# Kernel tuning notes

Measured on AMD Instinct MI355X. Metric: run time of the kernel, lower is better.

The kernel has to match this reference:

```python
import jax, jax.numpy as jnp
import numpy as np

DIM = 1024
HEADS = 16
DIM_HEADS = DIM // HEADS  # 64
DIM_HIDDEN = DIM_HEADS * HEADS


def setup_inputs() -> dict:
    key = jax.random.key(0)
    k1, k2, k3, k4, k5 = jax.random.split(key, 5)
    b, t = 2, 2048
    x = jax.random.normal(k1, (b, t, DIM), dtype=jnp.float32)
    # torch nn.Linear weights are [out_features, in_features]
    s = DIM ** -0.5
    W_q = jax.random.normal(k2, (DIM_HIDDEN, DIM), dtype=jnp.float32) * s
    W_kv = jax.random.normal(k3, (2 * DIM_HIDDEN, DIM), dtype=jnp.float32) * s
    W_out = jax.random.normal(k4, (DIM, DIM_HIDDEN), dtype=jnp.float32) * s
    b_out = jax.random.normal(k5, (DIM,), dtype=jnp.float32) * 0.01
    return {"x": x, "W_q": W_q, "W_kv": W_kv, "W_out": W_out, "b_out": b_out}


def reference(x, W_q, W_kv, W_out, b_out):
    b, t, d = x.shape
    h, e = HEADS, DIM_HEADS
    # projections (Linear: x @ W.T)
    q = jnp.einsum('btd,fd->btf', x, W_q)
    kv = jnp.einsum('btd,fd->btf', x, W_kv)
    k, v = jnp.split(kv, 2, axis=-1)
    # split heads -> (b, h, t, e)
    split = lambda z: z.reshape(b, t, h, e).transpose(0, 2, 1, 3)
    q, k, v = split(q), split(k), split(v)
    # scaled dot-product attention; original uses exp/sum/div softmax
    scores = jnp.einsum('bhqe,bhke->bhqk', q, k) * (e ** -0.5)
    attn = jax.nn.softmax(scores, axis=-1)
    out = jnp.einsum('bhqk,bhke->bhqe', attn, v)
    out = out.transpose(0, 2, 1, 3).reshape(b, t, h * e)
    return jnp.einsum('btf,df->btd', out, W_out) + b_out
```

## Files before the change

### kernel.cpp

```cpp
#include <hip/hip_runtime.h>
#include <hip/hip_bf16.h>

#define BB   2
#define TT   2048
#define DD   1024
#define HH   16
#define EE   64
#define BT   4096

typedef __attribute__((ext_vector_type(8))) short bf16x8;
typedef __attribute__((ext_vector_type(4))) float floatx4;
typedef __attribute__((ext_vector_type(16))) float floatx16;

__device__ __forceinline__ unsigned short f2bf(float f) {
  unsigned int x = __float_as_uint(f);
  x += 0x7fffu + ((x >> 16) & 1u);
  return (unsigned short)(x >> 16);
}
__device__ __forceinline__ unsigned int pack2u(float a, float b) {
  union { __hip_bfloat162 h; unsigned int u; } r;
  r.h = __float22bfloat162_rn(make_float2(a, b));
  return r.u;
}
__device__ __forceinline__ uint4 pack8(const float4& a, const float4& b) {
  union { uint4 u; __hip_bfloat162 h[4]; } r;
  r.h[0] = __float22bfloat162_rn(make_float2(a.x, a.y));
  r.h[1] = __float22bfloat162_rn(make_float2(a.z, a.w));
  r.h[2] = __float22bfloat162_rn(make_float2(b.x, b.y));
  r.h[3] = __float22bfloat162_rn(make_float2(b.z, b.w));
  return r.u;
}
__device__ __forceinline__ void ld16(unsigned short* lds, const unsigned short* g) {
  __builtin_amdgcn_global_load_lds(
      (const __attribute__((address_space(1))) unsigned int*)g,
      (__attribute__((address_space(3))) unsigned int*)lds, 16, 0, 0);
}

#define GX   524288
#define GWQ  131072
#define GWKV 262144
#define GWO  131072

__global__ __launch_bounds__(256) void convert_kernel(
    const float* __restrict__ X,  const float* __restrict__ Wq,
    const float* __restrict__ Wkv, const float* __restrict__ Wout,
    unsigned short* __restrict__ Xb, unsigned short* __restrict__ Wb,
    unsigned short* __restrict__ Wob) {
  int g = blockIdx.x * 256 + threadIdx.x;
  const float* src; unsigned short* dst; int gi;
  if (g < GX)                        { src = X;    dst = Xb;  gi = g; }
  else if ((g -= GX) < GWQ)          { src = Wq;   dst = Wb;  gi = g; }
  else if ((g -= GWQ) < GWKV)        { src = Wkv;  dst = Wb + (size_t)GWQ * 8; gi = g; }
  else                               { src = Wout; dst = Wob; gi = g - GWKV; }
  const float4* s4 = reinterpret_cast<const float4*>(src) + (size_t)gi * 2;
  float4 a = s4[0], b = s4[1];
  reinterpret_cast<uint4*>(dst)[gi] = pack8(a, b);
}

__global__ __launch_bounds__(256) void gemm_qkv_mfma(
    const unsigned short* __restrict__ Xb,
    const unsigned short* __restrict__ Wb,
    unsigned short* __restrict__ Qh,
    unsigned short* __restrict__ Kh,
    unsigned short* __restrict__ Vt) {
  __shared__ __align__(16) unsigned short smem[128 * 136];
  unsigned short* As = smem;
  unsigned short* Bs = smem + 128 * 64;
  const int tid  = threadIdx.x;
  const int lane = tid & 63, w = tid >> 6;
  const int wm = w >> 1, wn = w & 1;
  const int q = lane >> 4, c = lane & 15;
  const int bm0 = blockIdx.y * 128;
  const int bn0 = blockIdx.x * 128;
  const unsigned short* Ag = Xb + (size_t)bm0 * DD;
  const unsigned short* Bg = Wb + (size_t)bn0 * DD;

  floatx4 acc[4][4];
#pragma unroll
  for (int i = 0; i < 4; ++i)
#pragma unroll
    for (int j = 0; j < 4; ++j) acc[i][j] = (floatx4){0.f, 0.f, 0.f, 0.f};

  int prow[4], pch[4];
#pragma unroll
  for (int t = 0; t < 4; ++t) {
    int s = (w * 4 + t) * 64 + lane;
    prow[t] = s >> 3;
    pch[t]  = (s & 7) ^ (prow[t] & 7);
  }
  int aoff[4][2], boff[4][2];
#pragma unroll
  for (int i = 0; i < 4; ++i)
#pragma unroll
    for (int h = 0; h < 2; ++h) {
      aoff[i][h] = (wm * 64 + i * 16 + c) * 64 + (((q + h * 4) ^ (c & 7)) << 3);
      boff[i][h] = (wn * 64 + i * 16 + c) * 64 + (((q + h * 4) ^ (c & 7)) << 3);
    }

  for (int kk = 0; kk < DD; kk += 64) {
    __syncthreads();
#pragma unroll
    for (int t = 0; t < 4; ++t) {
      int i = w * 4 + t;
      ld16(&As[i * 512], &Ag[(size_t)prow[t] * DD + kk + pch[t] * 8]);
      ld16(&Bs[i * 512], &Bg[(size_t)prow[t] * DD + kk + pch[t] * 8]);
    }
    __syncthreads();
    bf16x8 af[4][2], bfr[4][2];
#pragma unroll
    for (int i = 0; i < 4; ++i)
#pragma unroll
      for (int h = 0; h < 2; ++h) {
        af[i][h]  = *reinterpret_cast<const bf16x8*>(&As[aoff[i][h]]);
        bfr[i][h] = *reinterpret_cast<const bf16x8*>(&Bs[boff[i][h]]);
      }
#pragma unroll
    for (int i = 0; i < 4; ++i)
#pragma unroll
      for (int j = 0; j < 4; ++j) {
        acc[i][j] = __builtin_amdgcn_mfma_f32_16x16x32_bf16(af[i][0], bfr[j][0], acc[i][j], 0, 0, 0);
        acc[i][j] = __builtin_amdgcn_mfma_f32_16x16x32_bf16(af[i][1], bfr[j][1], acc[i][j], 0, 0, 0);
      }
  }

  const int region = bn0 >> 10;
  if (region < 2) {
    const float scl = (region == 0) ? 0.18033688011112042f : 1.0f;
    __syncthreads();
    unsigned short* tb = smem;
#pragma unroll
    for (int i = 0; i < 4; ++i) {
#pragma unroll
      for (int j = 0; j < 4; ++j) {
        int n  = wn * 64 + j * 16 + c;
        int m0 = wm * 64 + i * 16 + q * 4;
#pragma unroll
        for (int reg = 0; reg < 4; ++reg)
          tb[(m0 + reg) * 136 + n] = f2bf(acc[i][j][reg] * scl);
      }
    }
    __syncthreads();
    unsigned short* dst = (region == 0) ? Qh : Kh;
    const int b   = bm0 >> 11;
    const int t0  = bm0 & 2047;
    const int nb0 = bn0 & 1023;
    const int oct = tid & 15;
    const int nb  = nb0 + oct * 8;
    const int h   = nb >> 6, e = nb & 63;
#pragma unroll
    for (int it = 0; it < 8; ++it) {
      int tr = it * 16 + (tid >> 4);
      uint4 vv = *reinterpret_cast<const uint4*>(&tb[tr * 136 + oct * 8]);
      *reinterpret_cast<uint4*>(
          &dst[((size_t)((b * HH + h) * TT + t0 + tr)) * EE + e]) = vv;
    }
  } else {
    __syncthreads();
    unsigned short* tb = smem;
#pragma unroll
    for (int i = 0; i < 4; ++i) {
#pragma unroll
      for (int j = 0; j < 4; ++j) {
        int nl = wn * 64 + j * 16 + c;
        int ml = wm * 64 + i * 16 + q * 4;
        ushort4 pk;
        pk.x = f2bf(acc[i][j][0]);
        pk.y = f2bf(acc[i][j][1]);
        pk.z = f2bf(acc[i][j][2]);
        pk.w = f2bf(acc[i][j][3]);
        *reinterpret_cast<ushort4*>(&tb[nl * 136 + ml]) = pk;
      }
    }
    __syncthreads();
    const int b  = bm0 >> 11;
    const int t0 = bm0 & 2047;
    const int nb0 = bn0 & 1023;
    const int lr = tid & 15;
#pragma unroll
    for (int it = 0; it < 8; ++it) {
      int nl = it * 16 + (tid >> 4);
      int nb = nb0 + nl;
      int h = nb >> 6, e = nb & 63;
      uint4 vv = *reinterpret_cast<const uint4*>(&tb[nl * 136 + lr * 8]);
      *reinterpret_cast<uint4*>(
          &Vt[((size_t)(b * HH + h) * EE + e) * TT + t0 + lr * 8]) = vv;
    }
  }
}

#define NKT 32

#define ATILE(P, PREF, VMC)                                                    \
  do {                                                                         \
    if (PREF) {                                                                \
      _Pragma("unroll")                                                        \
      for (int t = 0; t < 4; ++t) {                                            \
        ld16(&Kbuf[((P) ^ 1) * 4096 + (t * 2 + w) * 512], kpre[t]);            \
        kpre[t] += 4096;                                                       \
        ld16(&Vbuf[((P) ^ 1) * 4096 + (t * 2 + w) * 512], vpre[t]);            \
        vpre[t] += 64;                                                         \
      }                                                                        \
    }                                                                          \
    asm volatile("s_waitcnt vmcnt(" VMC ")" ::: "memory");                     \
    asm volatile("s_barrier" ::: "memory");                                    \
    bf16x8 kf[2][4];                                                           \
    _Pragma("unroll")                                                          \
    for (int nt = 0; nt < 2; ++nt)                                             \
      _Pragma("unroll")                                                        \
      for (int kc = 0; kc < 4; ++kc)                                           \
        kf[nt][kc] = *reinterpret_cast<const bf16x8*>(                         \
            &Kbuf[(P) * 4096 + koff[nt][kc]]);                                 \
    floatx16 sacc[2];                                                          \
    __builtin_amdgcn_s_setprio(1);                                             \
    _Pragma("unroll")                                                          \
    for (int nt = 0; nt < 2; ++nt) {                                           \
      sacc[nt] = __builtin_amdgcn_mfma_f32_32x32x16_bf16(kf[nt][0], qf[0], zf, 0, 0, 0); \
      _Pragma("unroll")                                                        \
      for (int kc = 1; kc < 4; ++kc)                                           \
        sacc[nt] = __builtin_amdgcn_mfma_f32_32x32x16_bf16(kf[nt][kc], qf[kc], sacc[nt], 0, 0, 0); \
    }                                                                          \
    __builtin_amdgcn_s_setprio(0);                                             \
    unsigned int pp[2][8];                                                     \
    _Pragma("unroll")                                                          \
    for (int nt = 0; nt < 2; ++nt)                                             \
      _Pragma("unroll")                                                        \
      for (int r = 0; r < 8; ++r) {                                            \
        float e0 = __builtin_amdgcn_exp2f(sacc[nt][2 * r]);                    \
        float e1 = __builtin_amdgcn_exp2f(sacc[nt][2 * r + 1]);                \
        pp[nt][r] = pack2u(e0, e1);                                            \
      }                                                                        \
    __builtin_amdgcn_s_setprio(1);                                             \
    _Pragma("unroll")                                                          \
    for (int nt = 0; nt < 2; ++nt)                                             \
      _Pragma("unroll")                                                        \
      for (int kcp = 0; kcp < 2; ++kcp) {                                      \
        union { unsigned int u[4]; bf16x8 v; } pf;                             \
        pf.u[0] = pp[nt][4 * kcp + 0]; pf.u[1] = pp[nt][4 * kcp + 1];          \
        pf.u[2] = pp[nt][4 * kcp + 2]; pf.u[3] = pp[nt][4 * kcp + 3];          \
        lacc = __builtin_amdgcn_mfma_f32_32x32x16_bf16(pf.v, onesf.v, lacc, 0, 0, 0); \
        _Pragma("unroll")                                                      \
        for (int eh = 0; eh < 2; ++eh) {                                       \
          const int cc = nt * 4 + 2 * kcp;                                     \
          uint2 v0 = *reinterpret_cast<const uint2*>(                          \
              &Vbuf[(P) * 4096 + voff[eh][cc]]);                               \
          uint2 v1 = *reinterpret_cast<const uint2*>(                          \
              &Vbuf[(P) * 4096 + voff[eh][cc + 1]]);                           \
          union { unsigned int u[4]; bf16x8 v; } vf;                           \
          vf.u[0] = v0.x; vf.u[1] = v0.y; vf.u[2] = v1.x; vf.u[3] = v1.y;      \
          o_acc[eh] = __builtin_amdgcn_mfma_f32_32x32x16_bf16(pf.v, vf.v, o_acc[eh], 0, 0, 0); \
        }                                                                      \
      }                                                                        \
    __builtin_amdgcn_s_setprio(0);                                             \
    asm volatile("s_barrier" ::: "memory");                                    \
  } while (0)

__global__ __launch_bounds__(128) void attn_kernel(
    const unsigned short* __restrict__ Qh,
    const unsigned short* __restrict__ Kh,
    const unsigned short* __restrict__ Vtg,
    unsigned short* __restrict__ Aw) {
  __shared__ __align__(16) unsigned short smem[16384];

  const int tid  = threadIdx.x;
  const int lane = tid & 63;
  const int w    = tid >> 6;
  const int n31  = lane & 31;
  const int g    = lane >> 5;

  const int flat = blockIdx.y * 32 + blockIdx.x;
  const int idx  = flat >> 3;
  const int bh   = (flat & 7) * 4 + (idx >> 5);
  const int qt   = idx & 31;
  const size_t base = (size_t)bh * TT * EE;
  const unsigned short* Qp = Qh + base + (size_t)(qt * 64 + w * 32) * EE;
  const unsigned short* Kp = Kh + base;
  const unsigned short* Vp = Vtg + base;

  unsigned short* Kbuf = smem;
  unsigned short* Vbuf = smem + 8192;

  union { unsigned int u[4]; bf16x8 v; } onesf;
  onesf.u[0] = 0x3F803F80u; onesf.u[1] = 0x3F803F80u;
  onesf.u[2] = 0x3F803F80u; onesf.u[3] = 0x3F803F80u;

  const floatx16 zf = (floatx16)(0.0f);

  bf16x8 qf[4];
#pragma unroll
  for (int kc = 0; kc < 4; ++kc)
    qf[kc] = *reinterpret_cast<const bf16x8*>(
        &Qp[(size_t)n31 * EE + kc * 16 + g * 8]);

  int srow[4], sch[4];
#pragma unroll
  for (int t = 0; t < 4; ++t) {
    int s = (t * 2 + w) * 64 + lane;
    srow[t] = s >> 3;
    sch[t]  = (s & 7) ^ (srow[t] & 7);
  }

  int koff[2][4];
#pragma unroll
  for (int nt = 0; nt < 2; ++nt) {
    const int krow = nt * 32 + n31;
#pragma unroll
    for (int kc = 0; kc < 4; ++kc)
      koff[nt][kc] = krow * 64 + (((kc * 2 + g) ^ (krow & 7)) << 3);
  }
  int voff[2][8];
#pragma unroll
  for (int eh = 0; eh < 2; ++eh) {
    const int vrow = eh * 32 + n31;
#pragma unroll
    for (int cc = 0; cc < 8; ++cc)
      voff[eh][cc] = vrow * 64 + ((cc ^ (vrow & 7)) << 3) + g * 4;
  }

  const unsigned short* kpre[4];
  const unsigned short* vpre[4];
#pragma unroll
  for (int t = 0; t < 4; ++t) {
    kpre[t] = Kp + (size_t)(64 + srow[t]) * EE + sch[t] * 8;
    vpre[t] = Vp + (size_t)srow[t] * TT + 64 + sch[t] * 8;
  }

  floatx16 o_acc[2];
  o_acc[0] = (floatx16)(0.0f);
  o_acc[1] = (floatx16)(0.0f);
  floatx16 lacc = (floatx16)(0.0f);

#pragma unroll
  for (int t = 0; t < 4; ++t) {
    ld16(&Kbuf[(t * 2 + w) * 512], Kp + (size_t)srow[t] * EE + sch[t] * 8);
    ld16(&Vbuf[(t * 2 + w) * 512], Vp + (size_t)srow[t] * TT + sch[t] * 8);
  }

  for (int kt2 = 0; kt2 < 15; ++kt2) {
    ATILE(0, true, "8");
    ATILE(1, true, "8");
  }
  ATILE(0, true, "8");
  ATILE(1, false, "0");

  const int b = bh >> 4, h = bh & 15;
#pragma unroll
  for (int eh = 0; eh < 2; ++eh)
#pragma unroll
    for (int reg = 0; reg < 16; ++reg) {
      int qrl = (reg & 3) + 8 * (reg >> 2) + 4 * g;
      int t = qt * 64 + w * 32 + qrl;
      Aw[((size_t)(b * TT + t)) * DD + h * EE + eh * 32 + n31] =
          f2bf(o_acc[eh][reg] * (1.0f / lacc[reg]));
    }
}

__global__ __launch_bounds__(256) void gemm_out_mfma(
    const unsigned short* __restrict__ A,
    const unsigned short* __restrict__ Wob,
    const float* __restrict__ bias,
    float* __restrict__ out) {
  __shared__ __align__(16) unsigned short As[128 * 64];
  __shared__ __align__(16) unsigned short Bs[64 * 64];
  const int tid  = threadIdx.x;
  const int lane = tid & 63, w = tid >> 6;
  const int wm = w >> 1, wn = w & 1;
  const int q = lane >> 4, c = lane & 15;
  const int bm0 = blockIdx.y * 128;
  const int bn0 = blockIdx.x * 64;
  const unsigned short* Ag = A + (size_t)bm0 * DD;
  const unsigned short* Bg = Wob + (size_t)bn0 * DD;

  floatx4 acc[4][2];
#pragma unroll
  for (int i = 0; i < 4; ++i)
#pragma unroll
    for (int j = 0; j < 2; ++j) acc[i][j] = (floatx4){0.f, 0.f, 0.f, 0.f};

  int parow[4], pach[4];
#pragma unroll
  for (int t = 0; t < 4; ++t) {
    int s = (w * 4 + t) * 64 + lane;
    parow[t] = s >> 3;
    pach[t]  = (s & 7) ^ (parow[t] & 7);
  }
  int pbrow[2], pbch[2];
#pragma unroll
  for (int t = 0; t < 2; ++t) {
    int s = (w * 2 + t) * 64 + lane;
    pbrow[t] = s >> 3;
    pbch[t]  = (s & 7) ^ (pbrow[t] & 7);
  }

  for (int kk = 0; kk < DD; kk += 64) {
    __syncthreads();
#pragma unroll
    for (int t = 0; t < 4; ++t)
      ld16(&As[(w * 4 + t) * 512], &Ag[(size_t)parow[t] * DD + kk + pach[t] * 8]);
#pragma unroll
    for (int t = 0; t < 2; ++t)
      ld16(&Bs[(w * 2 + t) * 512], &Bg[(size_t)pbrow[t] * DD + kk + pbch[t] * 8]);
    __syncthreads();
    bf16x8 af[4][2], bfr[2][2];
#pragma unroll
    for (int h = 0; h < 2; ++h) {
      int ksw = ((q + h * 4) ^ (c & 7)) << 3;
#pragma unroll
      for (int i = 0; i < 4; ++i)
        af[i][h] = *reinterpret_cast<const bf16x8*>(&As[(wm * 64 + i * 16 + c) * 64 + ksw]);
#pragma unroll
      for (int j = 0; j < 2; ++j)
        bfr[j][h] = *reinterpret_cast<const bf16x8*>(&Bs[(wn * 32 + j * 16 + c) * 64 + ksw]);
    }
#pragma unroll
    for (int i = 0; i < 4; ++i)
#pragma unroll
      for (int j = 0; j < 2; ++j) {
        acc[i][j] = __builtin_amdgcn_mfma_f32_16x16x32_bf16(af[i][0], bfr[j][0], acc[i][j], 0, 0, 0);
        acc[i][j] = __builtin_amdgcn_mfma_f32_16x16x32_bf16(af[i][1], bfr[j][1], acc[i][j], 0, 0, 0);
      }
  }

#pragma unroll
  for (int i = 0; i < 4; ++i) {
#pragma unroll
    for (int j = 0; j < 2; ++j) {
      int n = bn0 + wn * 32 + j * 16 + c;
      float bv = bias[n];
#pragma unroll
      for (int reg = 0; reg < 4; ++reg) {
        int m = bm0 + wm * 64 + i * 16 + q * 4 + reg;
        out[(size_t)m * DD + n] = acc[i][j][reg] + bv;
      }
    }
  }
}

extern "C" void kernel_launch(void* const* d_in, const int* in_sizes, int n_in,
                              void* d_out, int out_size, void* d_ws, size_t ws_size,
                              hipStream_t stream) {
  const float* X    = (const float*)d_in[0];
  const float* Wq   = (const float*)d_in[1];
  const float* Wkv  = (const float*)d_in[2];
  const float* Wout = (const float*)d_in[3];
  const float* bout = (const float*)d_in[4];
  float* out = (float*)d_out;

  unsigned short* Qh  = (unsigned short*)d_ws;
  unsigned short* Kh  = Qh + (size_t)BT * DD;
  unsigned short* Vt  = Kh + (size_t)BT * DD;
  unsigned short* Aw  = Vt + (size_t)BT * DD;
  unsigned short* Xb  = Aw;
  unsigned short* Wb  = Aw + (size_t)BT * DD;
  unsigned short* Wob = Wb + (size_t)3 * 1024 * DD;

  convert_kernel<<<dim3(4096), 256, 0, stream>>>(X, Wq, Wkv, Wout, Xb, Wb, Wob);
  gemm_qkv_mfma<<<dim3(24, 32), 256, 0, stream>>>(Xb, Wb, Qh, Kh, Vt);
  attn_kernel<<<dim3(32, 32), 128, 0, stream>>>(Qh, Kh, Vt, Aw);
  gemm_out_mfma<<<dim3(16, 32), 256, 0, stream>>>(Aw, Wob, bout, out);
}
```

Measured before the change: 194.4 us.

## Stage V tiles through registers into a padded LDS layout

V tiles are now loaded from global memory into registers and written to LDS with a padded row stride of 68 elements, replacing the XOR-swizzled direct global-to-LDS loads. The V-operand reads in the PV MFMA loop use plain padded offsets. The aim is to cut LDS bank conflicts on the 8-byte V fragment reads. In exchange it adds VGPR pressure, explicit ds_write instructions and an extra vmcnt/lgkmcnt wait inside each tile, so the V load latency has to be hidden within a single tile's compute.

```diff
diff --git a/kernel.cpp b/kernel.cpp
--- a/kernel.cpp
+++ b/kernel.cpp
@@ -189,16 +189,20 @@
 }
 
 #define NKT 32
+#define VST 68
 
 #define ATILE(P, PREF, VMC)                                                    \
   do {                                                                         \
     if (PREF) {                                                                \
       _Pragma("unroll")                                                        \
       for (int t = 0; t < 4; ++t) {                                            \
+        vreg[t] = *reinterpret_cast<const uint4*>(vpre[t]);                    \
+        vpre[t] += 64;                                                         \
+      }                                                                        \
+      _Pragma("unroll")                                                        \
+      for (int t = 0; t < 4; ++t) {                                            \
         ld16(&Kbuf[((P) ^ 1) * 4096 + (t * 2 + w) * 512], kpre[t]);            \
         kpre[t] += 4096;                                                       \
-        ld16(&Vbuf[((P) ^ 1) * 4096 + (t * 2 + w) * 512], vpre[t]);            \
-        vpre[t] += 64;                                                         \
       }                                                                        \
     }                                                                          \
     asm volatile("s_waitcnt vmcnt(" VMC ")" ::: "memory");                     \
@@ -242,15 +246,25 @@
         for (int eh = 0; eh < 2; ++eh) {                                       \
           const int cc = nt * 4 + 2 * kcp;                                     \
           uint2 v0 = *reinterpret_cast<const uint2*>(                          \
-              &Vbuf[(P) * 4096 + voff[eh][cc]]);                               \
+              &Vbuf[(P) * 4352 + voff[eh][cc]]);                               \
           uint2 v1 = *reinterpret_cast<const uint2*>(                          \
-              &Vbuf[(P) * 4096 + voff[eh][cc + 1]]);                           \
+              &Vbuf[(P) * 4352 + voff[eh][cc + 1]]);                           \
           union { unsigned int u[4]; bf16x8 v; } vf;                           \
           vf.u[0] = v0.x; vf.u[1] = v0.y; vf.u[2] = v1.x; vf.u[3] = v1.y;      \
           o_acc[eh] = __builtin_amdgcn_mfma_f32_32x32x16_bf16(pf.v, vf.v, o_acc[eh], 0, 0, 0); \
         }                                                                      \
       }                                                                        \
     __builtin_amdgcn_s_setprio(0);                                             \
+    if (PREF) {                                                                \
+      asm volatile("s_waitcnt vmcnt(4)" ::: "memory");                         \
+      _Pragma("unroll")                                                        \
+      for (int t = 0; t < 4; ++t) {                                            \
+        unsigned short* vd = &Vbuf[((P) ^ 1) * 4352 + vwoff[t]];               \
+        *reinterpret_cast<uint2*>(vd)     = make_uint2(vreg[t].x, vreg[t].y);  \
+        *reinterpret_cast<uint2*>(vd + 4) = make_uint2(vreg[t].z, vreg[t].w);  \
+      }                                                                        \
+      asm volatile("s_waitcnt lgkmcnt(0)" ::: "memory");                       \
+    }                                                                          \
     asm volatile("s_barrier" ::: "memory");                                    \
   } while (0)
 
@@ -259,7 +273,7 @@
     const unsigned short* __restrict__ Kh,
     const unsigned short* __restrict__ Vtg,
     unsigned short* __restrict__ Aw) {
-  __shared__ __align__(16) unsigned short smem[16384];
+  __shared__ __align__(16) unsigned short smem[16896];
 
   const int tid  = threadIdx.x;
   const int lane = tid & 63;
@@ -291,12 +305,14 @@
     qf[kc] = *reinterpret_cast<const bf16x8*>(
         &Qp[(size_t)n31 * EE + kc * 16 + g * 8]);
 
-  int srow[4], sch[4];
+  int srow[4], sch[4], voct[4], vwoff[4];
 #pragma unroll
   for (int t = 0; t < 4; ++t) {
     int s = (t * 2 + w) * 64 + lane;
     srow[t] = s >> 3;
     sch[t]  = (s & 7) ^ (srow[t] & 7);
+    voct[t] = s & 7;
+    vwoff[t] = srow[t] * VST + voct[t] * 8;
   }
 
   int koff[2][4];
@@ -313,7 +329,7 @@
     const int vrow = eh * 32 + n31;
 #pragma unroll
     for (int cc = 0; cc < 8; ++cc)
-      voff[eh][cc] = vrow * 64 + ((cc ^ (vrow & 7)) << 3) + g * 4;
+      voff[eh][cc] = vrow * VST + cc * 8 + g * 4;
   }
 
   const unsigned short* kpre[4];
@@ -321,7 +337,7 @@
 #pragma unroll
   for (int t = 0; t < 4; ++t) {
     kpre[t] = Kp + (size_t)(64 + srow[t]) * EE + sch[t] * 8;
-    vpre[t] = Vp + (size_t)srow[t] * TT + 64 + sch[t] * 8;
+    vpre[t] = Vp + (size_t)srow[t] * TT + 64 + voct[t] * 8;
   }
 
   floatx16 o_acc[2];
@@ -329,11 +345,23 @@
   o_acc[1] = (floatx16)(0.0f);
   floatx16 lacc = (floatx16)(0.0f);
 
+  uint4 vreg[4];
+
+#pragma unroll
+  for (int t = 0; t < 4; ++t)
+    vreg[t] = *reinterpret_cast<const uint4*>(
+        Vp + (size_t)srow[t] * TT + voct[t] * 8);
+#pragma unroll
+  for (int t = 0; t < 4; ++t)
+    ld16(&Kbuf[(t * 2 + w) * 512], Kp + (size_t)srow[t] * EE + sch[t] * 8);
+  asm volatile("s_waitcnt vmcnt(4)" ::: "memory");
 #pragma unroll
   for (int t = 0; t < 4; ++t) {
-    ld16(&Kbuf[(t * 2 + w) * 512], Kp + (size_t)srow[t] * EE + sch[t] * 8);
-    ld16(&Vbuf[(t * 2 + w) * 512], Vp + (size_t)srow[t] * TT + sch[t] * 8);
-  }
+    unsigned short* vd = &Vbuf[vwoff[t]];
+    *reinterpret_cast<uint2*>(vd)     = make_uint2(vreg[t].x, vreg[t].y);
+    *reinterpret_cast<uint2*>(vd + 4) = make_uint2(vreg[t].z, vreg[t].w);
+  }
+  asm volatile("s_waitcnt lgkmcnt(0)" ::: "memory");
 
   for (int kt2 = 0; kt2 < 15; ++kt2) {
     ATILE(0, true, "8");
```

Result: no change. 196.5 us (median of 2 runs) (+1.1%).
